# Kernel optimization log

Hardware: AMD Instinct MI355X
Metric: run time of the kernel (lower is better)

## Reference

```python
import jax, jax.numpy as jnp
import numpy as np

N_NODES = 10000
N_EDGES = 640000
D = 128


def setup_inputs() -> dict:
    key = jax.random.key(0)
    k1, k2, k3, k4 = jax.random.split(key, 4)
    X = jax.random.normal(k1, (N_NODES, D), dtype=jnp.float32)
    Y = jax.random.normal(k2, (N_EDGES, D), dtype=jnp.float32)
    # nn.Linear(in, out, bias=False): weight shape (out, in), y = Y @ W.T
    W = jax.random.normal(k3, (D, D), dtype=jnp.float32) * (1.0 / np.sqrt(D))
    edge_index = jax.random.randint(k4, (N_EDGES, 2), 0, N_NODES, dtype=jnp.int64)
    return {"X": X, "Y": Y, "W": W, "edge_index": edge_index}


def reference(X, Y, W, edge_index):
    # Edge transform: (E, d_in) @ (d_in, d_out) -> (E, d_out)
    Y_prime = jnp.einsum('ei,oi->eo', Y, W)
    # Scatter-add transformed edge features to source nodes
    src = edge_index[:, 0]
    agg = jax.ops.segment_sum(Y_prime, src, num_segments=X.shape[0])  # (N, d_out)
    # Residual + activation
    X_prime = jax.nn.relu(X + agg)
    return (X_prime, Y_prime)
```

## Files before the change

### kernel.cpp

```cpp
#include <hip/hip_runtime.h>

#define N_NODES 10000
#define N_EDGES 640000
#define DD 128
#define MAIN_BLOCKS 7500

typedef __attribute__((ext_vector_type(8))) short short8;
typedef __attribute__((ext_vector_type(8))) float f32x8;
typedef __attribute__((ext_vector_type(4))) float f32x4;
typedef __attribute__((ext_vector_type(2))) float f32x2;

__device__ __forceinline__ unsigned pack_bf2(float lo, float hi) {
  return __builtin_amdgcn_perm(__float_as_uint(hi), __float_as_uint(lo), 0x07060302u);
}

__device__ __forceinline__ void stage_w256(const float* __restrict__ W,
                                           short8* lwr) {
  const int tid = threadIdx.x;
#pragma unroll
  for (int t = 0; t < 8; ++t) {
    int s = t * 256 + tid;
    f32x8 v = *(const f32x8*)(W + (size_t)s * 8);
    short8 av;
    unsigned* au = (unsigned*)&av;
    au[0] = pack_bf2(v[0], v[1]);
    au[1] = pack_bf2(v[2], v[3]);
    au[2] = pack_bf2(v[4], v[5]);
    au[3] = pack_bf2(v[6], v[7]);
    int j = s >> 4;
    int c = s & 15;
    lwr[(j << 4) | (c ^ (j & 7))] = av;
  }
  __syncthreads();
}

__device__ __forceinline__ void gemm_chunk(const float* __restrict__ Y,
                                           float* __restrict__ Yp,
                                           const short8* lwr, int chunk) {
  const int wid  = threadIdx.x >> 6;
  const int lane = threadIdx.x & 63;
  const int l15  = lane & 15;
  const int lg   = lane >> 4;
  const int koff = lg * 8;
  const int row  = chunk * 64 + wid * 16 + l15;

  const float* yr = Y + (size_t)row * DD;
  short8 a[4];
#pragma unroll
  for (int kk = 0; kk < 4; ++kk) {
    f32x8 v = *(const f32x8*)(yr + kk * 32 + koff);
    short8 av;
    unsigned* au = (unsigned*)&av;
    au[0] = pack_bf2(v[0], v[1]);
    au[1] = pack_bf2(v[2], v[3]);
    au[2] = pack_bf2(v[4], v[5]);
    au[3] = pack_bf2(v[6], v[7]);
    a[kk] = av;
  }

  f32x4 acc[8];
#pragma unroll
  for (int nt = 0; nt < 8; ++nt)
    acc[nt] = (f32x4){0.f, 0.f, 0.f, 0.f};

#pragma unroll
  for (int nt = 0; nt < 8; ++nt) {
    const int j = nt * 16 + l15;
#pragma unroll
    for (int kk = 0; kk < 4; ++kk) {
      const int kc = kk * 4 + lg;
      short8 b = lwr[(j << 4) | (kc ^ (j & 7))];
      acc[nt] = __builtin_amdgcn_mfma_f32_16x16x32_bf16(b, a[kk], acc[nt], 0, 0, 0);
    }
  }

  float* orow = Yp + (size_t)row * DD + lg * 4;
#pragma unroll
  for (int nt = 0; nt < 8; ++nt)
    __builtin_nontemporal_store(acc[nt], (f32x4*)(orow + nt * 16));
}

__global__ __launch_bounds__(256) void k_zero(int* __restrict__ count) {
  const int i = blockIdx.x * 256 + threadIdx.x;
  if (i < N_NODES) count[i] = 0;
}

__global__ __launch_bounds__(256, 2) void k_hist_gemm(
    const int* __restrict__ EI, int* __restrict__ count,
    const float* __restrict__ Y, const float* __restrict__ W,
    float* __restrict__ Yp) {
  __shared__ short8 lwr[2048];
  const int e = blockIdx.x * 256 + threadIdx.x;
  atomicAdd(&count[EI[2 * e]], 1);
  stage_w256(W, lwr);
  gemm_chunk(Y, Yp, lwr, blockIdx.x);
}

__global__ __launch_bounds__(1024) void k_scan(const int* __restrict__ count,
                                               int* __restrict__ rowptr,
                                               int* __restrict__ cursor) {
  __shared__ int part[1024];
  const int tid = threadIdx.x;
  const int base = tid * 10;
  int local[10];
  int s = 0;
#pragma unroll
  for (int i = 0; i < 10; ++i) {
    const int idx = base + i;
    const int v = (idx < N_NODES) ? count[idx] : 0;
    local[i] = s;
    s += v;
  }
  part[tid] = s;
  __syncthreads();
  for (int off = 1; off < 1024; off <<= 1) {
    int v = 0;
    if (tid >= off) v = part[tid - off];
    __syncthreads();
    if (tid >= off) part[tid] += v;
    __syncthreads();
  }
  const int excl = (tid > 0) ? part[tid - 1] : 0;
#pragma unroll
  for (int i = 0; i < 10; ++i) {
    const int idx = base + i;
    if (idx < N_NODES) {
      const int r = excl + local[i];
      rowptr[idx] = r;
      cursor[idx] = r;
    }
  }
  if (tid == 1023) rowptr[N_NODES] = part[1023];
}

__global__ __launch_bounds__(256, 2) void k_fill_gemm(
    const int* __restrict__ EI, int* __restrict__ cursor,
    int* __restrict__ col,
    const float* __restrict__ Y, const float* __restrict__ W,
    float* __restrict__ Yp) {
  __shared__ short8 lwr[2048];
  const int e = blockIdx.x * 256 + threadIdx.x;
  const int s = EI[2 * e];
  const int pos = atomicAdd(&cursor[s], 1);
  col[pos] = e;
  stage_w256(W, lwr);
  gemm_chunk(Y, Yp, lwr, 2500 + blockIdx.x);
}

__global__ __launch_bounds__(256, 2) void k_main(
    const float* __restrict__ Y,
    const float* __restrict__ W,
    const int* __restrict__ rowptr,
    const int* __restrict__ col,
    float* __restrict__ Yp,
    float* __restrict__ segY) {
  __shared__ short8 lwr[2048];
  const int role = blockIdx.x % 3;
  const int grp  = blockIdx.x / 3;
  const int wid  = threadIdx.x >> 6;
  const int lane = threadIdx.x & 63;

  if (role == 0) {
    const int node = grp * 4 + wid;
    const size_t co = 2 * (size_t)lane;
    const int b  = rowptr[node];
    const int en = rowptr[node + 1];
    f32x2 acc = (f32x2){0.f, 0.f};
    int i = b;
    for (; i + 16 <= en; i += 16) {
      f32x2 v0 = *(const f32x2*)(Y + (size_t)col[i]      * DD + co);
      f32x2 v1 = *(const f32x2*)(Y + (size_t)col[i + 1]  * DD + co);
      f32x2 v2 = *(const f32x2*)(Y + (size_t)col[i + 2]  * DD + co);
      f32x2 v3 = *(const f32x2*)(Y + (size_t)col[i + 3]  * DD + co);
      f32x2 v4 = *(const f32x2*)(Y + (size_t)col[i + 4]  * DD + co);
      f32x2 v5 = *(const f32x2*)(Y + (size_t)col[i + 5]  * DD + co);
      f32x2 v6 = *(const f32x2*)(Y + (size_t)col[i + 6]  * DD + co);
      f32x2 v7 = *(const f32x2*)(Y + (size_t)col[i + 7]  * DD + co);
      f32x2 v8 = *(const f32x2*)(Y + (size_t)col[i + 8]  * DD + co);
      f32x2 v9 = *(const f32x2*)(Y + (size_t)col[i + 9]  * DD + co);
      f32x2 va = *(const f32x2*)(Y + (size_t)col[i + 10] * DD + co);
      f32x2 vb = *(const f32x2*)(Y + (size_t)col[i + 11] * DD + co);
      f32x2 vc = *(const f32x2*)(Y + (size_t)col[i + 12] * DD + co);
      f32x2 vd = *(const f32x2*)(Y + (size_t)col[i + 13] * DD + co);
      f32x2 ve = *(const f32x2*)(Y + (size_t)col[i + 14] * DD + co);
      f32x2 vf = *(const f32x2*)(Y + (size_t)col[i + 15] * DD + co);
      acc += v0; acc += v1; acc += v2; acc += v3;
      acc += v4; acc += v5; acc += v6; acc += v7;
      acc += v8; acc += v9; acc += va; acc += vb;
      acc += vc; acc += vd; acc += ve; acc += vf;
    }
    for (; i < en; ++i) {
      acc += *(const f32x2*)(Y + (size_t)col[i] * DD + co);
    }
    *(f32x2*)(segY + (size_t)node * DD + co) = acc;
    return;
  }

  stage_w256(W, lwr);
  gemm_chunk(Y, Yp, lwr, 5000 + grp * 2 + (role - 1));
}

__global__ __launch_bounds__(256, 2) void k_small(
    const float* __restrict__ segY,
    const float* __restrict__ W,
    const float* __restrict__ X,
    float* __restrict__ Xp) {
  __shared__ short8 lwr[2048];
  stage_w256(W, lwr);
  const int wid  = threadIdx.x >> 6;
  const int lane = threadIdx.x & 63;
  const int l15  = lane & 15;
  const int lg   = lane >> 4;
  const int koff = lg * 8;
  const int rbase = blockIdx.x * 128 + wid * 32;

  short8 a[2][4];
#pragma unroll
  for (int mt = 0; mt < 2; ++mt) {
    int row = rbase + mt * 16 + l15;
    if (row > N_NODES - 1) row = N_NODES - 1;
    const float* sr = segY + (size_t)row * DD + koff;
#pragma unroll
    for (int kk = 0; kk < 4; ++kk) {
      f32x8 v = *(const f32x8*)(sr + kk * 32);
      short8 av;
      unsigned* au = (unsigned*)&av;
      au[0] = pack_bf2(v[0], v[1]);
      au[1] = pack_bf2(v[2], v[3]);
      au[2] = pack_bf2(v[4], v[5]);
      au[3] = pack_bf2(v[6], v[7]);
      a[mt][kk] = av;
    }
  }

  f32x4 acc[2][8];
#pragma unroll
  for (int mt = 0; mt < 2; ++mt)
#pragma unroll
    for (int nt = 0; nt < 8; ++nt)
      acc[mt][nt] = (f32x4){0.f, 0.f, 0.f, 0.f};

#pragma unroll
  for (int nt = 0; nt < 8; ++nt) {
    const int j = nt * 16 + l15;
#pragma unroll
    for (int kk = 0; kk < 4; ++kk) {
      const int kc = kk * 4 + lg;
      short8 b = lwr[(j << 4) | (kc ^ (j & 7))];
      acc[0][nt] = __builtin_amdgcn_mfma_f32_16x16x32_bf16(b, a[0][kk], acc[0][nt], 0, 0, 0);
      acc[1][nt] = __builtin_amdgcn_mfma_f32_16x16x32_bf16(b, a[1][kk], acc[1][nt], 0, 0, 0);
    }
  }

#pragma unroll
  for (int mt = 0; mt < 2; ++mt) {
    const int row = rbase + mt * 16 + l15;
    if (row < N_NODES) {
      const float* xr   = X  + (size_t)row * DD + lg * 4;
      float*       orow = Xp + (size_t)row * DD + lg * 4;
#pragma unroll
      for (int nt = 0; nt < 8; ++nt) {
        f32x4 x = *(const f32x4*)(xr + nt * 16);
        f32x4 v = acc[mt][nt] + x;
        f32x4 r;
        r[0] = v[0] > 0.f ? v[0] : 0.f;
        r[1] = v[1] > 0.f ? v[1] : 0.f;
        r[2] = v[2] > 0.f ? v[2] : 0.f;
        r[3] = v[3] > 0.f ? v[3] : 0.f;
        *(f32x4*)(orow + nt * 16) = r;
      }
    }
  }
}

extern "C" void kernel_launch(void* const* d_in, const int* in_sizes, int n_in,
                              void* d_out, int out_size, void* d_ws, size_t ws_size,
                              hipStream_t stream) {
  const float* X  = (const float*)d_in[0];
  const float* Y  = (const float*)d_in[1];
  const float* W  = (const float*)d_in[2];
  const int*   EI = (const int*)d_in[3];

  float* Xp = (float*)d_out;
  float* Yp = Xp + (size_t)N_NODES * DD;

  int* w      = (int*)d_ws;
  int* count  = w;
  int* rowptr = w + 10000;
  int* cursor = w + 20001;
  int* col    = w + 30001;
  float* segY = (float*)(w + 670001 + 15);

  k_zero<<<(N_NODES + 255) / 256, 256, 0, stream>>>(count);
  k_hist_gemm<<<2500, 256, 0, stream>>>(EI, count, Y, W, Yp);
  k_scan<<<1, 1024, 0, stream>>>(count, rowptr, cursor);
  k_fill_gemm<<<2500, 256, 0, stream>>>(EI, cursor, col, Y, W, Yp);
  k_main<<<MAIN_BLOCKS, 256, 0, stream>>>(Y, W, rowptr, col, Yp, segY);
  k_small<<<(N_NODES + 127) / 128, 256, 0, stream>>>(segY, W, X, Xp);
}
```

Baseline: 275.3 us.

## Process two 64-row GEMM chunks per block and halve grid sizes

Each GEMM block now handles two 64-row chunks of Y, loading the second chunk's inputs while the MFMAs for the first chunk run. This amortises the per-block staging of W into LDS across twice the rows, so the histogram, fill and main kernels launch half as many GEMM blocks and each handles two edges per thread. It raises register pressure and lowers block-level parallelism, and in k_main the gather blocks now interleave 1:1 with GEMM blocks instead of 1:2.

```diff
diff --git a/kernel.cpp b/kernel.cpp
--- a/kernel.cpp
+++ b/kernel.cpp
@@ -3,7 +3,6 @@
 #define N_NODES 10000
 #define N_EDGES 640000
 #define DD 128
-#define MAIN_BLOCKS 7500
 
 typedef __attribute__((ext_vector_type(8))) short short8;
 typedef __attribute__((ext_vector_type(8))) float f32x8;
@@ -34,50 +33,76 @@
   __syncthreads();
 }
 
-__device__ __forceinline__ void gemm_chunk(const float* __restrict__ Y,
+__device__ __forceinline__ void pack_a(const f32x4* raw, short8* a) {
+#pragma unroll
+  for (int kk = 0; kk < 4; ++kk) {
+    f32x4 v0 = raw[kk * 2];
+    f32x4 v1 = raw[kk * 2 + 1];
+    short8 av;
+    unsigned* au = (unsigned*)&av;
+    au[0] = pack_bf2(v0[0], v0[1]);
+    au[1] = pack_bf2(v0[2], v0[3]);
+    au[2] = pack_bf2(v1[0], v1[1]);
+    au[3] = pack_bf2(v1[2], v1[3]);
+    a[kk] = av;
+  }
+}
+
+__device__ __forceinline__ void mfma_store(const short8* a, const short8* lwr,
                                            float* __restrict__ Yp,
-                                           const short8* lwr, int chunk) {
+                                           int row, int l15, int lg) {
+  f32x4 acc[8];
+#pragma unroll
+  for (int nt = 0; nt < 8; ++nt)
+    acc[nt] = (f32x4){0.f, 0.f, 0.f, 0.f};
+#pragma unroll
+  for (int nt = 0; nt < 8; ++nt) {
+    const int j = nt * 16 + l15;
+#pragma unroll
+    for (int kk = 0; kk < 4; ++kk) {
+      const int kc = kk * 4 + lg;
+      short8 b = lwr[(j << 4) | (kc ^ (j & 7))];
+      acc[nt] = __builtin_amdgcn_mfma_f32_16x16x32_bf16(b, a[kk], acc[nt], 0, 0, 0);
+    }
+  }
+  float* orow = Yp + (size_t)row * DD + lg * 4;
+#pragma unroll
+  for (int nt = 0; nt < 8; ++nt)
+    __builtin_nontemporal_store(acc[nt], (f32x4*)(orow + nt * 16));
+}
+
+__device__ __forceinline__ void gemm_chunk2(const float* __restrict__ Y,
+                                            float* __restrict__ Yp,
+                                            const short8* lwr, int c0) {
   const int wid  = threadIdx.x >> 6;
   const int lane = threadIdx.x & 63;
   const int l15  = lane & 15;
   const int lg   = lane >> 4;
   const int koff = lg * 8;
-  const int row  = chunk * 64 + wid * 16 + l15;
-
-  const float* yr = Y + (size_t)row * DD;
+  const int row0 = c0 * 64 + wid * 16 + l15;
+
+  f32x4 raw[8];
+  const float* yr0 = Y + (size_t)row0 * DD + koff;
+#pragma unroll
+  for (int kk = 0; kk < 4; ++kk) {
+    raw[kk * 2]     = *(const f32x4*)(yr0 + kk * 32);
+    raw[kk * 2 + 1] = *(const f32x4*)(yr0 + kk * 32 + 4);
+  }
+
   short8 a[4];
+  pack_a(raw, a);
+
+  const float* yr1 = Y + (size_t)(row0 + 64) * DD + koff;
 #pragma unroll
   for (int kk = 0; kk < 4; ++kk) {
-    f32x8 v = *(const f32x8*)(yr + kk * 32 + koff);
-    short8 av;
-    unsigned* au = (unsigned*)&av;
-    au[0] = pack_bf2(v[0], v[1]);
-    au[1] = pack_bf2(v[2], v[3]);
-    au[2] = pack_bf2(v[4], v[5]);
-    au[3] = pack_bf2(v[6], v[7]);
-    a[kk] = av;
-  }
-
-  f32x4 acc[8];
-#pragma unroll
-  for (int nt = 0; nt < 8; ++nt)
-    acc[nt] = (f32x4){0.f, 0.f, 0.f, 0.f};
-
-#pragma unroll
-  for (int nt = 0; nt < 8; ++nt) {
-    const int j = nt * 16 + l15;
-#pragma unroll
-    for (int kk = 0; kk < 4; ++kk) {
-      const int kc = kk * 4 + lg;
-      short8 b = lwr[(j << 4) | (kc ^ (j & 7))];
-      acc[nt] = __builtin_amdgcn_mfma_f32_16x16x32_bf16(b, a[kk], acc[nt], 0, 0, 0);
-    }
-  }
-
-  float* orow = Yp + (size_t)row * DD + lg * 4;
-#pragma unroll
-  for (int nt = 0; nt < 8; ++nt)
-    __builtin_nontemporal_store(acc[nt], (f32x4*)(orow + nt * 16));
+    raw[kk * 2]     = *(const f32x4*)(yr1 + kk * 32);
+    raw[kk * 2 + 1] = *(const f32x4*)(yr1 + kk * 32 + 4);
+  }
+
+  mfma_store(a, lwr, Yp, row0, l15, lg);
+
+  pack_a(raw, a);
+  mfma_store(a, lwr, Yp, row0 + 64, l15, lg);
 }
 
 __global__ __launch_bounds__(256) void k_zero(int* __restrict__ count) {
@@ -90,10 +115,11 @@
     const float* __restrict__ Y, const float* __restrict__ W,
     float* __restrict__ Yp) {
   __shared__ short8 lwr[2048];
-  const int e = blockIdx.x * 256 + threadIdx.x;
+  const int e = blockIdx.x * 512 + threadIdx.x;
   atomicAdd(&count[EI[2 * e]], 1);
+  atomicAdd(&count[EI[2 * (e + 256)]], 1);
   stage_w256(W, lwr);
-  gemm_chunk(Y, Yp, lwr, blockIdx.x);
+  gemm_chunk2(Y, Yp, lwr, blockIdx.x * 2);
 }
 
 __global__ __launch_bounds__(1024) void k_scan(const int* __restrict__ count,
@@ -139,12 +165,20 @@
     const float* __restrict__ Y, const float* __restrict__ W,
     float* __restrict__ Yp) {
   __shared__ short8 lwr[2048];
-  const int e = blockIdx.x * 256 + threadIdx.x;
-  const int s = EI[2 * e];
-  const int pos = atomicAdd(&cursor[s], 1);
-  col[pos] = e;
+  const int e = blockIdx.x * 512 + threadIdx.x;
+  {
+    const int s = EI[2 * e];
+    const int pos = atomicAdd(&cursor[s], 1);
+    col[pos] = e;
+  }
+  {
+    const int e2 = e + 256;
+    const int s = EI[2 * e2];
+    const int pos = atomicAdd(&cursor[s], 1);
+    col[pos] = e2;
+  }
   stage_w256(W, lwr);
-  gemm_chunk(Y, Yp, lwr, 2500 + blockIdx.x);
+  gemm_chunk2(Y, Yp, lwr, 2500 + blockIdx.x * 2);
 }
 
 __global__ __launch_bounds__(256, 2) void k_main(
@@ -155,8 +189,8 @@
     float* __restrict__ Yp,
     float* __restrict__ segY) {
   __shared__ short8 lwr[2048];
-  const int role = blockIdx.x % 3;
-  const int grp  = blockIdx.x / 3;
+  const int role = blockIdx.x % 2;
+  const int grp  = blockIdx.x / 2;
   const int wid  = threadIdx.x >> 6;
   const int lane = threadIdx.x & 63;
 
@@ -197,7 +231,7 @@
   }
 
   stage_w256(W, lwr);
-  gemm_chunk(Y, Yp, lwr, 5000 + grp * 2 + (role - 1));
+  gemm_chunk2(Y, Yp, lwr, 5000 + grp * 2);
 }
 
 __global__ __launch_bounds__(256, 2) void k_small(
@@ -292,9 +326,9 @@
   float* segY = (float*)(w + 670001 + 15);
 
   k_zero<<<(N_NODES + 255) / 256, 256, 0, stream>>>(count);
-  k_hist_gemm<<<2500, 256, 0, stream>>>(EI, count, Y, W, Yp);
+  k_hist_gemm<<<1250, 256, 0, stream>>>(EI, count, Y, W, Yp);
   k_scan<<<1, 1024, 0, stream>>>(count, rowptr, cursor);
-  k_fill_gemm<<<2500, 256, 0, stream>>>(EI, cursor, col, Y, W, Yp);
-  k_main<<<MAIN_BLOCKS, 256, 0, stream>>>(Y, W, rowptr, col, Yp, segY);
+  k_fill_gemm<<<1250, 256, 0, stream>>>(EI, cursor, col, Y, W, Yp);
+  k_main<<<5000, 256, 0, stream>>>(Y, W, rowptr, col, Yp, segY);
   k_small<<<(N_NODES + 127) / 128, 256, 0, stream>>>(segY, W, X, Xp);
 }
```

After: 353.2 us. 1.28x slower.
